# Optimization experiments

Hardware: AMD Instinct MI355X
Metric: run time of the kernel (lower is better)

Reference implementation:

```python
import jax, jax.numpy as jnp
from jax import lax
import numpy as np

EPS = 0.15      # constraint_value_upper_bound (per-row box |y/c - 1| <= EPS)
DELTA = 0.05    # groups_constraint_upper_bound (per-group mean |y/c - 1| <= DELTA)
N_GROUPS = 8
N_ITERS = 300   # Dykstra iterations; converges to the exact QP projection

N, D, H1, H2, K = 65536, 512, 1024, 512, 1


def setup_inputs() -> dict:
    key = jax.random.key(0)
    ks = jax.random.split(key, 8)
    x = jax.random.normal(ks[0], (N, D), jnp.float32)
    W1 = jax.random.normal(ks[1], (D, H1), jnp.float32) / np.float32(np.sqrt(D))
    b1 = jnp.zeros((H1,), jnp.float32)
    W2 = jax.random.normal(ks[2], (H1, H2), jnp.float32) / np.float32(np.sqrt(H1))
    b2 = jnp.zeros((H2,), jnp.float32)
    Wf = jax.random.normal(ks[3], (H2, K), jnp.float32) / np.float32(np.sqrt(H2))
    bf = jnp.zeros((K,), jnp.float32)
    c = jax.random.uniform(ks[4], (N,), jnp.float32, 0.5, 2.0)
    # quantiles_price_tensor: q_i = (1/N) * #{k : c_k <= c_i}  (rank via searchsorted)
    q = jnp.searchsorted(jnp.sort(c), c, side='right').astype(jnp.float32) / N
    # group j covers q in [j/G, (j+1)/G]; assign boundary ties to the lower group
    g = jnp.clip(jnp.ceil(q * N_GROUPS).astype(jnp.int32) - 1, 0, N_GROUPS - 1)
    group_mask = jax.nn.one_hot(g, N_GROUPS, dtype=jnp.float32).T  # [G, N]
    return dict(x=x, W1=W1, b1=b1, W2=W2, b2=b2, Wf=Wf, bf=bf,
                constraint_constant=c, group_mask=group_mask)


def _project(y_u, c, group_mask):
    """Exact QP: min ||y - y_u||^2 s.t. |y_i/c_i - 1| <= EPS and
    |mean_{i in G_j}(y_i/c_i - 1)| <= DELTA, solved by Dykstra's alternating
    projections in z = y/c - 1 space under the weighted norm sum c_i^2 z_i^2."""
    w = c * c                                   # [N] weights of the norm
    z0 = y_u / c[:, None] - 1.0                 # [N, K]
    n = group_mask.sum(axis=1)                  # [G] group sizes
    a = group_mask / n[:, None]                 # [G, N] averaging rows
    denom = (a * a / w[None, :]).sum(axis=1)    # [G]  a^T W^{-1} a
    u = (a / w[None, :]) / denom[:, None]       # [G, N] weighted slab directions

    def proj_box(z):
        return jnp.clip(z, -EPS, EPS)

    def proj_grp(z):
        v = a @ z                               # [G, K] group means
        return z - u.T @ (v - jnp.clip(v, -DELTA, DELTA))

    def body(carry, _):
        z, p, q = carry
        zb = proj_box(z + p); p = z + p - zb
        zg = proj_grp(zb + q); q = zb + q - zg
        return (zg, p, q), None

    init = (z0, jnp.zeros_like(z0), jnp.zeros_like(z0))
    (z, _, _), _ = lax.scan(body, init, None, length=N_ITERS)
    return (z + 1.0) * c[:, None]


def reference(x, W1, b1, W2, b2, Wf, bf, constraint_constant, group_mask):
    h = jax.nn.relu(x @ W1 + b1)   # Dropout is identity in eval mode
    h = jax.nn.relu(h @ W2 + b2)
    y_u = h @ Wf + bf              # [N, 1] unconstrained predictions
    return _project(y_u, constraint_constant, group_mask)
```

## Files before the change

kernel.cpp:

```cpp
#include <hip/hip_runtime.h>
#include <hip/hip_bf16.h>

#define NROWS 65536
#define DIM   512
#define H1DIM 1024
#define H2DIM 512
#define EPSC  0.15f
#define DELTA 0.05f
#define NGRP  8
#define CAPG  16384

typedef __bf16 bf16x8 __attribute__((ext_vector_type(8)));
typedef float  f32x4  __attribute__((ext_vector_type(4)));

__device__ __forceinline__ void gload16(const void* g, void* lds) {
  __builtin_amdgcn_global_load_lds((__attribute__((address_space(1))) const unsigned int*)g,
                                   (__attribute__((address_space(3))) unsigned int*)lds,
                                   16, 0, 0);
}

__global__ void k_tcvt2(const float* __restrict__ W1, __bf16* __restrict__ w1t,
                        const float* __restrict__ W2, __bf16* __restrict__ w2t) {
  __shared__ float tile[32][33];
  const float* src; __bf16* dst; int R, C, bid;
  if (blockIdx.x < 512) { src = W1; dst = w1t; R = DIM;   C = H1DIM; bid = blockIdx.x; }
  else                  { src = W2; dst = w2t; R = H1DIM; C = H2DIM; bid = blockIdx.x - 512; }
  const int bx = C / 32;
  const int bi = (bid / bx) * 32;
  const int bj = (bid % bx) * 32;
  const int tx = threadIdx.x, ty = threadIdx.y;
  #pragma unroll
  for (int r = ty; r < 32; r += 8)
    tile[r][tx] = src[(size_t)(bi + r) * C + bj + tx];
  __syncthreads();
  #pragma unroll
  for (int r = ty; r < 32; r += 8)
    dst[(size_t)(bj + r) * R + bi + tx] = (__bf16)tile[tx][r];
}

__global__ __launch_bounds__(256) void k_cvt_x(const float4* __restrict__ x4,
                                               bf16x8* __restrict__ xb8, int n8,
                                               float* __restrict__ y_u, int zn,
                                               int* __restrict__ cnt) {
  const int stride = gridDim.x * blockDim.x;
  const int tid0 = blockIdx.x * blockDim.x + threadIdx.x;
  for (int i = tid0; i < n8; i += stride) {
    const float4 a = x4[2 * i];
    const float4 b = x4[2 * i + 1];
    bf16x8 v;
    v[0] = (__bf16)a.x; v[1] = (__bf16)a.y; v[2] = (__bf16)a.z; v[3] = (__bf16)a.w;
    v[4] = (__bf16)b.x; v[5] = (__bf16)b.y; v[6] = (__bf16)b.z; v[7] = (__bf16)b.w;
    xb8[i] = v;
  }
  for (int j = tid0; j < zn; j += stride) y_u[j] = 0.f;
  if (zn > 0 && tid0 < NGRP) cnt[tid0] = 0;
}


__global__ __launch_bounds__(512, 2) void k_gemm1(const __bf16* __restrict__ xb,
                                                  const __bf16* __restrict__ w1t,
                                                  const float* __restrict__ b1,
                                                  __bf16* __restrict__ h1) {
  __shared__ __align__(16) __bf16 As[2][256 * 64];
  __shared__ __align__(16) __bf16 Bs[2][256 * 64];
  const int tid = threadIdx.x;
  const int w = tid >> 6, l = tid & 63;
  const int mt   = (int)gridDim.x >> 2;
  const int mper = mt >> 3;
  const int xcd  = blockIdx.x & 7;
  const int idx  = blockIdx.x >> 3;
  const int brow = (xcd * mper + (idx >> 2)) * 256;
  const int bcol = (idx & 3) * 256;
  const int lr = l & 15, lk = l >> 4;
  const int wm = w >> 2, wn = w & 3;
  const int mbase = wm * 128, nbase = wn * 64;
  const int srow = w * 32 + (l >> 3);
  const int scol = (((l & 7) ^ ((l >> 3) & 7)) * 8);
  const int swz  = (lr & 7) << 4;
  const int NT = DIM / 64;
  f32x4 acc[8][4] = {};

  #define STAGE1(KT, BUF) do { \
    _Pragma("unroll") for (int t_ = 0; t_ < 4; ++t_) { \
      gload16(xb  + (size_t)(brow + srow + t_ * 8) * DIM + (KT) + scol, \
              As[BUF] + (w * 32 + t_ * 8) * 64); \
      gload16(w1t + (size_t)(bcol + srow + t_ * 8) * DIM + (KT) + scol, \
              Bs[BUF] + (w * 32 + t_ * 8) * 64); } } while (0)
  #define COMPUTE1(BUF) do { \
    _Pragma("unroll") for (int kk = 0; kk < 64; kk += 32) { \
      bf16x8 af[8], bq[4]; \
      _Pragma("unroll") for (int m = 0; m < 8; ++m) \
        af[m] = *(const bf16x8*)((const char*)(As[BUF]) + \
                 ((((mbase + m * 16 + lr) * 128) + kk * 2 + lk * 16) ^ swz)); \
      _Pragma("unroll") for (int nn = 0; nn < 4; ++nn) \
        bq[nn] = *(const bf16x8*)((const char*)(Bs[BUF]) + \
                 ((((nbase + nn * 16 + lr) * 128) + kk * 2 + lk * 16) ^ swz)); \
      __builtin_amdgcn_s_setprio(1); \
      _Pragma("unroll") for (int m = 0; m < 8; ++m) \
        _Pragma("unroll") for (int nn = 0; nn < 4; ++nn) \
          acc[m][nn] = __builtin_amdgcn_mfma_f32_16x16x32_bf16(af[m], bq[nn], acc[m][nn], 0, 0, 0); \
      __builtin_amdgcn_s_setprio(0); \
    } } while (0)

  STAGE1(0, 0);
  int cur = 0;
  for (int t = 0; t < NT - 1; ++t) {
    STAGE1((t + 1) * 64, cur ^ 1);
    asm volatile("s_waitcnt vmcnt(8)" ::: "memory");
    __builtin_amdgcn_s_barrier();
    COMPUTE1(cur);
    __builtin_amdgcn_s_barrier();
    cur ^= 1;
  }
  asm volatile("s_waitcnt vmcnt(0)" ::: "memory");
  __builtin_amdgcn_s_barrier();
  COMPUTE1(cur);

  #undef STAGE1
  #undef COMPUTE1

  #pragma unroll
  for (int nn = 0; nn < 4; ++nn) {
    const int col = bcol + nbase + nn * 16 + lr;
    const float bias = b1[col];
    #pragma unroll
    for (int m = 0; m < 8; ++m) {
      const int row = brow + mbase + m * 16 + lk * 4;
      #pragma unroll
      for (int j = 0; j < 4; ++j) {
        float v = acc[m][nn][j] + bias;
        v = fmaxf(v, 0.f);
        h1[(size_t)(row + j) * H1DIM + col] = (__bf16)v;
      }
    }
  }
}

__global__ __launch_bounds__(512, 2) void k_gemm2(const __bf16* __restrict__ h1,
                                                  const __bf16* __restrict__ w2t,
                                                  const float* __restrict__ b2,
                                                  const float* __restrict__ wf,
                                                  float* __restrict__ y_u) {
  __shared__ __align__(16) __bf16 As[2][256 * 64];
  __shared__ __align__(16) __bf16 Bs[2][256 * 64];
  __shared__ float yred[256];
  const int tid = threadIdx.x;
  const int w = tid >> 6, l = tid & 63;
  const int mt   = (int)gridDim.x >> 1;
  const int mper = mt >> 3;
  const int xcd  = blockIdx.x & 7;
  const int idx  = blockIdx.x >> 3;
  const int brow = (xcd * mper + (idx >> 1)) * 256;
  const int n0   = (idx & 1) * 256;
  const int lr = l & 15, lk = l >> 4;
  const int wm = w >> 2, wn = w & 3;
  const int mbase = wm * 128, nbase = wn * 64;
  const int srow = w * 32 + (l >> 3);
  const int scol = (((l & 7) ^ ((l >> 3) & 7)) * 8);
  const int swz  = (lr & 7) << 4;
  const int NT = H1DIM / 64;
  f32x4 acc[8][4] = {};

  #define STAGE2(KT, BUF) do { \
    _Pragma("unroll") for (int t_ = 0; t_ < 4; ++t_) { \
      gload16(h1  + (size_t)(brow + srow + t_ * 8) * H1DIM + (KT) + scol, \
              As[BUF] + (w * 32 + t_ * 8) * 64); \
      gload16(w2t + (size_t)(n0   + srow + t_ * 8) * H1DIM + (KT) + scol, \
              Bs[BUF] + (w * 32 + t_ * 8) * 64); } } while (0)
  #define COMPUTE2(BUF) do { \
    _Pragma("unroll") for (int kk = 0; kk < 64; kk += 32) { \
      bf16x8 af[8], bq[4]; \
      _Pragma("unroll") for (int m = 0; m < 8; ++m) \
        af[m] = *(const bf16x8*)((const char*)(As[BUF]) + \
                 ((((mbase + m * 16 + lr) * 128) + kk * 2 + lk * 16) ^ swz)); \
      _Pragma("unroll") for (int nn = 0; nn < 4; ++nn) \
        bq[nn] = *(const bf16x8*)((const char*)(Bs[BUF]) + \
                 ((((nbase + nn * 16 + lr) * 128) + kk * 2 + lk * 16) ^ swz)); \
      __builtin_amdgcn_s_setprio(1); \
      _Pragma("unroll") for (int m = 0; m < 8; ++m) \
        _Pragma("unroll") for (int nn = 0; nn < 4; ++nn) \
          acc[m][nn] = __builtin_amdgcn_mfma_f32_16x16x32_bf16(af[m], bq[nn], acc[m][nn], 0, 0, 0); \
      __builtin_amdgcn_s_setprio(0); \
    } } while (0)

  STAGE2(0, 0);
  int cur = 0;
  for (int t = 0; t < NT - 1; ++t) {
    STAGE2((t + 1) * 64, cur ^ 1);
    asm volatile("s_waitcnt vmcnt(8)" ::: "memory");
    __builtin_amdgcn_s_barrier();
    COMPUTE2(cur);
    __builtin_amdgcn_s_barrier();
    cur ^= 1;
  }
  asm volatile("s_waitcnt vmcnt(0)" ::: "memory");
  __builtin_amdgcn_s_barrier();
  COMPUTE2(cur);

  #undef STAGE2
  #undef COMPUTE2

  float yacc[8][4] = {};
  #pragma unroll
  for (int nn = 0; nn < 4; ++nn) {
    const int col = n0 + nbase + nn * 16 + lr;
    const float bias = b2[col];
    const float wfv = wf[col];
    #pragma unroll
    for (int m = 0; m < 8; ++m)
      #pragma unroll
      for (int j = 0; j < 4; ++j)
        yacc[m][j] += fmaxf(acc[m][nn][j] + bias, 0.f) * wfv;
  }
  #pragma unroll
  for (int m = 0; m < 8; ++m)
    #pragma unroll
    for (int j = 0; j < 4; ++j) {
      float v = yacc[m][j];
      v += __shfl_xor(v, 1, 64);
      v += __shfl_xor(v, 2, 64);
      v += __shfl_xor(v, 4, 64);
      v += __shfl_xor(v, 8, 64);
      yacc[m][j] = v;
    }
  if (tid < 256) yred[tid] = 0.f;
  __syncthreads();
  if (lr == 0) {
    #pragma unroll
    for (int m = 0; m < 8; ++m)
      #pragma unroll
      for (int j = 0; j < 4; ++j)
        atomicAdd(&yred[mbase + m * 16 + lk * 4 + j], yacc[m][j]);
  }
  __syncthreads();
  if (tid < 256) atomicAdd(&y_u[brow + tid], yred[tid]);
}

__global__ __launch_bounds__(256) void k_scatter(const float* __restrict__ y_u,
                                                 const float* __restrict__ c,
                                                 const float* __restrict__ mask,
                                                 const float* __restrict__ bfp,
                                                 float* __restrict__ z0c, float* __restrict__ iwc,
                                                 unsigned char* __restrict__ gidx,
                                                 int* __restrict__ cnt, int n) {
  __shared__ int lcnt[NGRP];
  __shared__ int lbase[NGRP];
  const float bf0 = bfp[0];
  const int tid = threadIdx.x;
  if (tid < NGRP) lcnt[tid] = 0;
  __syncthreads();
  const int i = blockIdx.x * blockDim.x + tid;
  int g = 0, slot_l = 0;
  float z0 = 0.f, iw = 0.f;
  if (i < n) {
    const float cv = c[i];
    z0 = (y_u[i] + bf0) / cv - 1.f;
    iw = 1.f / (cv * cv);
    #pragma unroll
    for (int j = 1; j < NGRP; ++j)
      if (mask[(size_t)j * NROWS + i] > 0.5f) g = j;
    slot_l = atomicAdd(&lcnt[g], 1);
    gidx[i] = (unsigned char)g;
  }
  __syncthreads();
  if (tid < NGRP) lbase[tid] = atomicAdd(&cnt[tid], lcnt[tid]);
  __syncthreads();
  if (i < n) {
    const int slot = lbase[g] + slot_l;
    if (slot < CAPG) {
      z0c[(size_t)g * CAPG + slot] = z0;
      iwc[(size_t)g * CAPG + slot] = iw;
    }
  }
}

__device__ __forceinline__ void red2(float& a, float& b, float* reda, float* redb, int tid) {
  #pragma unroll
  for (int o = 32; o > 0; o >>= 1) {
    a += __shfl_xor(a, o, 64);
    b += __shfl_xor(b, o, 64);
  }
  if ((tid & 63) == 0) { reda[tid >> 6] = a; redb[tid >> 6] = b; }
  __syncthreads();
  if (tid < 64) {
    float x = (tid < 16) ? reda[tid] : 0.f;
    float y = (tid < 16) ? redb[tid] : 0.f;
    #pragma unroll
    for (int o = 32; o > 0; o >>= 1) {
      x += __shfl_xor(x, o, 64);
      y += __shfl_xor(y, o, 64);
    }
    if (tid == 0) { reda[0] = x; redb[0] = y; }
  }
  __syncthreads();
  a = reda[0]; b = redb[0];
  __syncthreads();
}

__global__ __launch_bounds__(1024) void k_mu(const float* __restrict__ z0c,
                                             const float* __restrict__ iwc,
                                             const int* __restrict__ cnt,
                                             float* __restrict__ muarr) {
  __shared__ float reda[16], redb[16];
  const int g = blockIdx.x;
  const int tid = threadIdx.x;
  int n = cnt[g];
  if (n > CAPG) n = CAPG;
  if (n <= 0) { if (tid == 0) muarr[g] = 0.f; return; }
  float z0v[16], iwv[16];
  float hmax = -1e30f, hmin = 1e30f;
  #pragma unroll
  for (int t = 0; t < 16; ++t) {
    const int idx = t * 1024 + tid;
    if (idx < n) {
      const float z0 = z0c[(size_t)g * CAPG + idx];
      const float iw = iwc[(size_t)g * CAPG + idx];
      z0v[t] = z0; iwv[t] = iw;
      const float wv = 1.f / iw;
      hmax = fmaxf(hmax, (z0 + EPSC) * wv);
      hmin = fminf(hmin, (z0 - EPSC) * wv);
    } else { z0v[t] = 0.f; iwv[t] = 0.f; }
  }
  const float inv_n = 1.f / (float)n;
  #define EVAL2(MU, MS, DS) do { \
    float s_ = 0.f, d_ = 0.f; \
    _Pragma("unroll") for (int t_ = 0; t_ < 16; ++t_) { \
      float zz_ = z0v[t_] - (MU) * iwv[t_]; \
      if (zz_ > EPSC) zz_ = EPSC; \
      else if (zz_ < -EPSC) zz_ = -EPSC; \
      else d_ += iwv[t_]; \
      s_ += zz_; } \
    red2(s_, d_, reda, redb, tid); \
    MS = s_ * inv_n; DS = d_ * inv_n; \
  } while (0)
  float m0, d0;
  EVAL2(0.f, m0, d0);
  float mu = 0.f;
  if (fabsf(m0) > DELTA) {
    float hx = hmax, hn = -hmin;
    #pragma unroll
    for (int o = 32; o > 0; o >>= 1) {
      hx = fmaxf(hx, __shfl_xor(hx, o, 64));
      hn = fmaxf(hn, __shfl_xor(hn, o, 64));
    }
    if ((tid & 63) == 0) { reda[tid >> 6] = hx; redb[tid >> 6] = hn; }
    __syncthreads();
    if (tid < 64) {
      float x = (tid < 16) ? reda[tid] : -1e30f;
      float y = (tid < 16) ? redb[tid] : -1e30f;
      #pragma unroll
      for (int o = 32; o > 0; o >>= 1) {
        x = fmaxf(x, __shfl_xor(x, o, 64));
        y = fmaxf(y, __shfl_xor(y, o, 64));
      }
      if (tid == 0) { reda[0] = x; redb[0] = y; }
    }
    __syncthreads();
    const float hmax_r = reda[0], hmin_r = -redb[0];
    __syncthreads();
    float target, lo, hi;
    if (m0 > 0.f) { target = DELTA;  lo = 0.f;    hi = hmax_r; }
    else          { target = -DELTA; lo = hmin_r; hi = 0.f;    }
    mu = (d0 > 0.f) ? (m0 - target) / d0 : 0.5f * (lo + hi);
    if (!(mu > lo && mu < hi)) mu = 0.5f * (lo + hi);
    for (int it = 0; it < 9; ++it) {
      float mm, dd;
      EVAL2(mu, mm, dd);
      if (mm >= target) lo = mu; else hi = mu;
      float nm = (dd > 0.f) ? mu + (mm - target) / dd : 0.5f * (lo + hi);
      if (!(nm > lo && nm < hi)) nm = 0.5f * (lo + hi);
      mu = nm;
    }
  }
  if (tid == 0) muarr[g] = mu;
  #undef EVAL2
}

__global__ void k_y(const float* __restrict__ y_u, const float* __restrict__ c,
                    const float* __restrict__ bfp, const unsigned char* __restrict__ gidx,
                    const float* __restrict__ muarr, float* __restrict__ out, int n) {
  const float bf0 = bfp[0];
  int i = blockIdx.x * blockDim.x + threadIdx.x;
  const int stride = gridDim.x * blockDim.x;
  for (; i < n; i += stride) {
    const float cv = c[i];
    const float z0 = (y_u[i] + bf0) / cv - 1.f;
    const float mu = muarr[gidx[i]];
    const float z = fminf(fmaxf(z0 - mu / (cv * cv), -EPSC), EPSC);
    out[i] = (z + 1.f) * cv;
  }
}

extern "C" void kernel_launch(void* const* d_in, const int* in_sizes, int n_in,
                              void* d_out, int out_size, void* d_ws, size_t ws_size,
                              hipStream_t stream) {
  const float* x    = (const float*)d_in[0];
  const float* W1   = (const float*)d_in[1];
  const float* b1   = (const float*)d_in[2];
  const float* W2   = (const float*)d_in[3];
  const float* b2   = (const float*)d_in[4];
  const float* Wf   = (const float*)d_in[5];
  const float* bfp  = (const float*)d_in[6];
  const float* c    = (const float*)d_in[7];
  const float* mask = (const float*)d_in[8];
  float* out = (float*)d_out;

  char* ws = (char*)d_ws;
  size_t off = 0;
  auto alloc = [&](size_t bytes) -> void* {
    void* p = ws + off;
    off += (bytes + 255) & ~(size_t)255;
    return p;
  };
  __bf16* w1t = (__bf16*)alloc((size_t)H1DIM * DIM * 2);
  __bf16* w2t = (__bf16*)alloc((size_t)H2DIM * H1DIM * 2);
  float* y_u  = (float*)alloc((size_t)NROWS * 4);
  float* z0c  = (float*)alloc((size_t)NGRP * CAPG * 4);
  float* iwc  = (float*)alloc((size_t)NGRP * CAPG * 4);
  unsigned char* gidx = (unsigned char*)alloc(NROWS);
  int*   cnt  = (int*)alloc(NGRP * 4);
  float* muarr = (float*)alloc(NGRP * 4);
  const size_t fixed = off;

  size_t avail = (ws_size > fixed) ? (ws_size - fixed) : 0;
  long long rc = (long long)(avail / ((size_t)(DIM * 2 + H1DIM * 2)));
  rc &= ~2047LL;
  if (rc > NROWS) rc = NROWS;
  if (rc < 2048) rc = 2048;
  const int rows_chunk = (int)rc;
  __bf16* xb = (__bf16*)(ws + fixed);
  __bf16* h1 = (__bf16*)(ws + fixed + (size_t)rows_chunk * DIM * 2);

  k_tcvt2<<<dim3(1024), dim3(32, 8), 0, stream>>>(W1, w1t, W2, w2t);

  bool first = true;
  for (int r0 = 0; r0 < NROWS; r0 += rows_chunk) {
    const int Mc = (NROWS - r0 < rows_chunk) ? (NROWS - r0) : rows_chunk;
    const int mtiles = Mc / 256;
    const int n8 = Mc * (DIM / 8);
    int cblocks = (n8 + 255) / 256; if (cblocks > 2048) cblocks = 2048;
    k_cvt_x<<<dim3(cblocks), dim3(256), 0, stream>>>(
        (const float4*)(x + (size_t)r0 * DIM), (bf16x8*)xb, n8,
        y_u, first ? NROWS : 0, cnt);
    first = false;
    k_gemm1<<<dim3(mtiles * 4), dim3(512), 0, stream>>>(xb, w1t, b1, h1);
    k_gemm2<<<dim3(mtiles * 2), dim3(512), 0, stream>>>(h1, w2t, b2, Wf, y_u + r0);
  }

  k_scatter<<<dim3((NROWS + 255) / 256), dim3(256), 0, stream>>>(y_u, c, mask, bfp, z0c, iwc, gidx, cnt, NROWS);
  k_mu<<<dim3(NGRP), dim3(1024), 0, stream>>>(z0c, iwc, cnt, muarr);
  k_y<<<dim3(256), dim3(256), 0, stream>>>(y_u, c, bfp, gidx, muarr, out, NROWS);
}
```

Baseline: 231.0 us.

## Split GEMM tiles into quadrant phases interleaving LDS reads, prefetch and MFMA

Both bf16 GEMM kernels now split each 256x256 block tile into four 128x128 quadrants, with a new warp-to-quadrant mapping. Each K-step runs in four phases that interleave LDS fragment reads, global-to-LDS prefetch of the next half-tiles, and MFMA groups. The aim is to overlap global loads and LDS reads with matrix math and to cut register pressure from holding all fragments at once. In exchange there are more barriers per K-step and finer vmcnt waits, and correctness depends on that wait ordering being right.

```diff
diff --git a/kernel.cpp b/kernel.cpp
--- a/kernel.cpp
+++ b/kernel.cpp
@@ -56,6 +56,30 @@
   if (zn > 0 && tid0 < NGRP) cnt[tid0] = 0;
 }
 
+
+#define RD_A(ARR, BUF, MH) do { \
+  _Pragma("unroll") for (int kk_ = 0; kk_ < 2; ++kk_) \
+    _Pragma("unroll") for (int m_ = 0; m_ < 4; ++m_) \
+      aR[kk_][m_] = *(const bf16x8*)((const char*)(ARR[BUF]) + \
+        (((((MH) * 128 + wm * 64 + m_ * 16 + lr) * 128) + kk_ * 64 + lk * 16) ^ swz)); \
+} while (0)
+#define RD_B(ARR, BUF, NH) do { \
+  _Pragma("unroll") for (int kk_ = 0; kk_ < 2; ++kk_) \
+    _Pragma("unroll") for (int n_ = 0; n_ < 2; ++n_) \
+      bR[(NH) * 2 + n_][kk_] = *(const bf16x8*)((const char*)(ARR[BUF]) + \
+        (((((NH) * 128 + wn * 32 + n_ * 16 + lr) * 128) + kk_ * 64 + lk * 16) ^ swz)); \
+} while (0)
+#define MFMA_Q(MH, NH) do { \
+  __builtin_amdgcn_s_setprio(1); \
+  _Pragma("unroll") for (int kk_ = 0; kk_ < 2; ++kk_) \
+    _Pragma("unroll") for (int m_ = 0; m_ < 4; ++m_) \
+      _Pragma("unroll") for (int n_ = 0; n_ < 2; ++n_) \
+        acc[(MH) * 4 + m_][(NH) * 2 + n_] = __builtin_amdgcn_mfma_f32_16x16x32_bf16( \
+            aR[kk_][m_], bR[(NH) * 2 + n_][kk_], acc[(MH) * 4 + m_][(NH) * 2 + n_], 0, 0, 0); \
+  __builtin_amdgcn_s_setprio(0); \
+} while (0)
+#define VM4 asm volatile("s_waitcnt vmcnt(4)" ::: "memory")
+#define BAR __builtin_amdgcn_s_barrier()
 
 __global__ __launch_bounds__(512, 2) void k_gemm1(const __bf16* __restrict__ xb,
                                                   const __bf16* __restrict__ w1t,
@@ -73,64 +97,63 @@
   const int bcol = (idx & 3) * 256;
   const int lr = l & 15, lk = l >> 4;
   const int wm = w >> 2, wn = w & 3;
-  const int mbase = wm * 128, nbase = wn * 64;
-  const int srow = w * 32 + (l >> 3);
-  const int scol = (((l & 7) ^ ((l >> 3) & 7)) * 8);
-  const int swz  = (lr & 7) << 4;
+  const int srow8 = w * 8 + (l >> 3);
+  const int scol  = ((l & 7) ^ ((l >> 3) & 7)) * 8;
+  const int swz   = (lr & 7) << 4;
   const int NT = DIM / 64;
   f32x4 acc[8][4] = {};
-
-  #define STAGE1(KT, BUF) do { \
-    _Pragma("unroll") for (int t_ = 0; t_ < 4; ++t_) { \
-      gload16(xb  + (size_t)(brow + srow + t_ * 8) * DIM + (KT) + scol, \
-              As[BUF] + (w * 32 + t_ * 8) * 64); \
-      gload16(w1t + (size_t)(bcol + srow + t_ * 8) * DIM + (KT) + scol, \
-              Bs[BUF] + (w * 32 + t_ * 8) * 64); } } while (0)
-  #define COMPUTE1(BUF) do { \
-    _Pragma("unroll") for (int kk = 0; kk < 64; kk += 32) { \
-      bf16x8 af[8], bq[4]; \
-      _Pragma("unroll") for (int m = 0; m < 8; ++m) \
-        af[m] = *(const bf16x8*)((const char*)(As[BUF]) + \
-                 ((((mbase + m * 16 + lr) * 128) + kk * 2 + lk * 16) ^ swz)); \
-      _Pragma("unroll") for (int nn = 0; nn < 4; ++nn) \
-        bq[nn] = *(const bf16x8*)((const char*)(Bs[BUF]) + \
-                 ((((nbase + nn * 16 + lr) * 128) + kk * 2 + lk * 16) ^ swz)); \
-      __builtin_amdgcn_s_setprio(1); \
-      _Pragma("unroll") for (int m = 0; m < 8; ++m) \
-        _Pragma("unroll") for (int nn = 0; nn < 4; ++nn) \
-          acc[m][nn] = __builtin_amdgcn_mfma_f32_16x16x32_bf16(af[m], bq[nn], acc[m][nn], 0, 0, 0); \
-      __builtin_amdgcn_s_setprio(0); \
-    } } while (0)
-
-  STAGE1(0, 0);
+  bf16x8 aR[2][4], bR[4][2];
+
+  #define STG_A1(KT, BUF, H) do { \
+    gload16(xb + (size_t)(brow + (H) * 128 + srow8) * DIM + (KT) + scol, \
+            As[BUF] + ((H) * 128 + w * 8) * 64); \
+    gload16(xb + (size_t)(brow + (H) * 128 + 64 + srow8) * DIM + (KT) + scol, \
+            As[BUF] + ((H) * 128 + 64 + w * 8) * 64); } while (0)
+  #define STG_B1(KT, BUF, H) do { \
+    gload16(w1t + (size_t)(bcol + (H) * 128 + srow8) * DIM + (KT) + scol, \
+            Bs[BUF] + ((H) * 128 + w * 8) * 64); \
+    gload16(w1t + (size_t)(bcol + (H) * 128 + 64 + srow8) * DIM + (KT) + scol, \
+            Bs[BUF] + ((H) * 128 + 64 + w * 8) * 64); } while (0)
+
+  STG_A1(0, 0, 0); STG_B1(0, 0, 0); STG_B1(0, 0, 1); STG_A1(0, 0, 1);
+  VM4; BAR;
   int cur = 0;
-  for (int t = 0; t < NT - 1; ++t) {
-    STAGE1((t + 1) * 64, cur ^ 1);
-    asm volatile("s_waitcnt vmcnt(8)" ::: "memory");
-    __builtin_amdgcn_s_barrier();
-    COMPUTE1(cur);
-    __builtin_amdgcn_s_barrier();
+  for (int t = 0; t < NT; ++t) {
+    const int ktn = (t + 1) * 64;
+    const bool pre = (t + 1 < NT);
+    RD_A(As, cur, 0); RD_B(Bs, cur, 0);
+    if (pre) { STG_A1(ktn, cur ^ 1, 0); VM4; }
+    else     { asm volatile("s_waitcnt vmcnt(2)" ::: "memory"); }
+    BAR;
+    MFMA_Q(0, 0);
+    RD_B(Bs, cur, 1);
+    if (pre) { STG_B1(ktn, cur ^ 1, 0); VM4; }
+    else     { asm volatile("s_waitcnt vmcnt(0)" ::: "memory"); }
+    BAR;
+    MFMA_Q(0, 1);
+    RD_A(As, cur, 1);
+    if (pre) STG_B1(ktn, cur ^ 1, 1);
+    BAR;
+    MFMA_Q(1, 1);
+    if (pre) { STG_A1(ktn, cur ^ 1, 1); VM4; }
+    BAR;
+    MFMA_Q(1, 0);
     cur ^= 1;
   }
-  asm volatile("s_waitcnt vmcnt(0)" ::: "memory");
-  __builtin_amdgcn_s_barrier();
-  COMPUTE1(cur);
-
-  #undef STAGE1
-  #undef COMPUTE1
+  #undef STG_A1
+  #undef STG_B1
 
   #pragma unroll
   for (int nn = 0; nn < 4; ++nn) {
-    const int col = bcol + nbase + nn * 16 + lr;
+    const int col = bcol + (nn >> 1) * 128 + wn * 32 + (nn & 1) * 16 + lr;
     const float bias = b1[col];
     #pragma unroll
     for (int m = 0; m < 8; ++m) {
-      const int row = brow + mbase + m * 16 + lk * 4;
+      const int row = brow + (m >> 2) * 128 + wm * 64 + (m & 3) * 16 + lk * 4;
       #pragma unroll
       for (int j = 0; j < 4; ++j) {
         float v = acc[m][nn][j] + bias;
-        v = fmaxf(v, 0.f);
-        h1[(size_t)(row + j) * H1DIM + col] = (__bf16)v;
+        h1[(size_t)(row + j) * H1DIM + col] = (__bf16)fmaxf(v, 0.f);
       }
     }
   }
@@ -154,56 +177,56 @@
   const int n0   = (idx & 1) * 256;
   const int lr = l & 15, lk = l >> 4;
   const int wm = w >> 2, wn = w & 3;
-  const int mbase = wm * 128, nbase = wn * 64;
-  const int srow = w * 32 + (l >> 3);
-  const int scol = (((l & 7) ^ ((l >> 3) & 7)) * 8);
-  const int swz  = (lr & 7) << 4;
+  const int srow8 = w * 8 + (l >> 3);
+  const int scol  = ((l & 7) ^ ((l >> 3) & 7)) * 8;
+  const int swz   = (lr & 7) << 4;
   const int NT = H1DIM / 64;
   f32x4 acc[8][4] = {};
-
-  #define STAGE2(KT, BUF) do { \
-    _Pragma("unroll") for (int t_ = 0; t_ < 4; ++t_) { \
-      gload16(h1  + (size_t)(brow + srow + t_ * 8) * H1DIM + (KT) + scol, \
-              As[BUF] + (w * 32 + t_ * 8) * 64); \
-      gload16(w2t + (size_t)(n0   + srow + t_ * 8) * H1DIM + (KT) + scol, \
-              Bs[BUF] + (w * 32 + t_ * 8) * 64); } } while (0)
-  #define COMPUTE2(BUF) do { \
-    _Pragma("unroll") for (int kk = 0; kk < 64; kk += 32) { \
-      bf16x8 af[8], bq[4]; \
-      _Pragma("unroll") for (int m = 0; m < 8; ++m) \
-        af[m] = *(const bf16x8*)((const char*)(As[BUF]) + \
-                 ((((mbase + m * 16 + lr) * 128) + kk * 2 + lk * 16) ^ swz)); \
-      _Pragma("unroll") for (int nn = 0; nn < 4; ++nn) \
-        bq[nn] = *(const bf16x8*)((const char*)(Bs[BUF]) + \
-                 ((((nbase + nn * 16 + lr) * 128) + kk * 2 + lk * 16) ^ swz)); \
-      __builtin_amdgcn_s_setprio(1); \
-      _Pragma("unroll") for (int m = 0; m < 8; ++m) \
-        _Pragma("unroll") for (int nn = 0; nn < 4; ++nn) \
-          acc[m][nn] = __builtin_amdgcn_mfma_f32_16x16x32_bf16(af[m], bq[nn], acc[m][nn], 0, 0, 0); \
-      __builtin_amdgcn_s_setprio(0); \
-    } } while (0)
-
-  STAGE2(0, 0);
+  bf16x8 aR[2][4], bR[4][2];
+
+  #define STG_A2(KT, BUF, H) do { \
+    gload16(h1 + (size_t)(brow + (H) * 128 + srow8) * H1DIM + (KT) + scol, \
+            As[BUF] + ((H) * 128 + w * 8) * 64); \
+    gload16(h1 + (size_t)(brow + (H) * 128 + 64 + srow8) * H1DIM + (KT) + scol, \
+            As[BUF] + ((H) * 128 + 64 + w * 8) * 64); } while (0)
+  #define STG_B2(KT, BUF, H) do { \
+    gload16(w2t + (size_t)(n0 + (H) * 128 + srow8) * H1DIM + (KT) + scol, \
+            Bs[BUF] + ((H) * 128 + w * 8) * 64); \
+    gload16(w2t + (size_t)(n0 + (H) * 128 + 64 + srow8) * H1DIM + (KT) + scol, \
+            Bs[BUF] + ((H) * 128 + 64 + w * 8) * 64); } while (0)
+
+  STG_A2(0, 0, 0); STG_B2(0, 0, 0); STG_B2(0, 0, 1); STG_A2(0, 0, 1);
+  VM4; BAR;
   int cur = 0;
-  for (int t = 0; t < NT - 1; ++t) {
-    STAGE2((t + 1) * 64, cur ^ 1);
-    asm volatile("s_waitcnt vmcnt(8)" ::: "memory");
-    __builtin_amdgcn_s_barrier();
-    COMPUTE2(cur);
-    __builtin_amdgcn_s_barrier();
+  for (int t = 0; t < NT; ++t) {
+    const int ktn = (t + 1) * 64;
+    const bool pre = (t + 1 < NT);
+    RD_A(As, cur, 0); RD_B(Bs, cur, 0);
+    if (pre) { STG_A2(ktn, cur ^ 1, 0); VM4; }
+    else     { asm volatile("s_waitcnt vmcnt(2)" ::: "memory"); }
+    BAR;
+    MFMA_Q(0, 0);
+    RD_B(Bs, cur, 1);
+    if (pre) { STG_B2(ktn, cur ^ 1, 0); VM4; }
+    else     { asm volatile("s_waitcnt vmcnt(0)" ::: "memory"); }
+    BAR;
+    MFMA_Q(0, 1);
+    RD_A(As, cur, 1);
+    if (pre) STG_B2(ktn, cur ^ 1, 1);
+    BAR;
+    MFMA_Q(1, 1);
+    if (pre) { STG_A2(ktn, cur ^ 1, 1); VM4; }
+    BAR;
+    MFMA_Q(1, 0);
     cur ^= 1;
   }
-  asm volatile("s_waitcnt vmcnt(0)" ::: "memory");
-  __builtin_amdgcn_s_barrier();
-  COMPUTE2(cur);
-
-  #undef STAGE2
-  #undef COMPUTE2
+  #undef STG_A2
+  #undef STG_B2
 
   float yacc[8][4] = {};
   #pragma unroll
   for (int nn = 0; nn < 4; ++nn) {
-    const int col = n0 + nbase + nn * 16 + lr;
+    const int col = n0 + (nn >> 1) * 128 + wn * 32 + (nn & 1) * 16 + lr;
     const float bias = b2[col];
     const float wfv = wf[col];
     #pragma unroll
@@ -230,11 +253,17 @@
     for (int m = 0; m < 8; ++m)
       #pragma unroll
       for (int j = 0; j < 4; ++j)
-        atomicAdd(&yred[mbase + m * 16 + lk * 4 + j], yacc[m][j]);
+        atomicAdd(&yred[(m >> 2) * 128 + wm * 64 + (m & 3) * 16 + lk * 4 + j], yacc[m][j]);
   }
   __syncthreads();
   if (tid < 256) atomicAdd(&y_u[brow + tid], yred[tid]);
 }
+
+#undef RD_A
+#undef RD_B
+#undef MFMA_Q
+#undef VM4
+#undef BAR
 
 __global__ __launch_bounds__(256) void k_scatter(const float* __restrict__ y_u,
                                                  const float* __restrict__ c,
```

Result: faster. 220.8 us (median of 3 runs) (-4.4%).
